# Kernel tuning notes

Hardware: AMD Instinct MI355X
Metric: run time of the kernel (lower is better)

## Reference

```python
import jax, jax.numpy as jnp
import numpy as np

NUM_HEADS = 16
HEAD_DIM = 64
MAX_TIME = 10000


def apply_rope(x):
    """Interleaved RoPE, faithful to apply_rotary_encoding with the _rope_kernel.

    The NxN kernel maps pairs (x0, x1) -> (-x1, x0); we do it with a reshape
    instead of the dense matmul for efficiency (same math).
    x: [b, t, h, d]
    """
    b, t, h, d = x.shape
    pos = jnp.arange(t, dtype=jnp.float32)                         # [t]
    freq_seq = jnp.arange(d // 2, dtype=jnp.float32) / (d // 2)
    inv_freq = jnp.repeat(jnp.float32(MAX_TIME) ** (-freq_seq), 2)  # [d], interleaved
    theta = pos[:, None] * inv_freq[None, :]                        # [t, d]
    pairs = x.reshape(b, t, h, d // 2, 2)
    x_rot = jnp.stack([-pairs[..., 1], pairs[..., 0]], axis=-1).reshape(b, t, h, d)
    cos = jnp.cos(theta).astype(x.dtype)[None, :, None, :]
    sin = jnp.sin(theta).astype(x.dtype)[None, :, None, :]
    return x * cos + x_rot * sin


def setup_inputs() -> dict:
    key = jax.random.key(0)
    ks = jax.random.split(key, 6)
    B, T, E = 8, 1024, 1024
    H = NUM_HEADS * HEAD_DIM
    s = 0.02  # typical init scale for bias-free Linear weights
    return {
        "inputs_q": jax.random.normal(ks[0], (B, T, E), jnp.float32),
        "inputs_kv": jax.random.normal(ks[1], (B, T, E), jnp.float32),
        "w_q": jax.random.normal(ks[2], (E, H), jnp.float32) * s,
        "w_k": jax.random.normal(ks[3], (E, H), jnp.float32) * s,
        "w_v": jax.random.normal(ks[4], (E, H), jnp.float32) * s,
        "w_o": jax.random.normal(ks[5], (H, E), jnp.float32) * s,
    }


def reference(inputs_q, inputs_kv, w_q, w_k, w_v, w_o):
    b, t, e = inputs_q.shape
    q = (inputs_q @ w_q).reshape(b, t, NUM_HEADS, HEAD_DIM)   # [b,t,h,d]
    k = (inputs_kv @ w_k).reshape(b, -1, NUM_HEADS, HEAD_DIM)  # [b,T,h,d]
    v = (inputs_kv @ w_v).reshape(b, -1, NUM_HEADS, HEAD_DIM)
    q = apply_rope(q)
    k = apply_rope(k)
    logits = jnp.einsum('bthd,bThd->bhtT', q, k) * (1.0 / jnp.sqrt(jnp.float32(HEAD_DIM)))
    attn = jax.nn.softmax(logits, axis=-1)                    # [b,h,t,T]
    out = jnp.einsum('bhtT,bThd->bthd', attn, v).reshape(b, t, NUM_HEADS * HEAD_DIM)
    return out @ w_o                                          # [b,t,e]
```

## Files before the change

kernel.cpp:

```cpp
#include <hip/hip_runtime.h>
#include <math.h>


typedef __attribute__((ext_vector_type(8))) short bf16x8;
typedef __attribute__((ext_vector_type(4))) float f32x4;
typedef __attribute__((ext_vector_type(16))) float f32x16;

#define LOG2E 1.44269504f
#define QSCALE (0.125f * LOG2E)

__device__ __forceinline__ ushort f2bf(float f) {
    union { float f; uint32_t u; } v; v.f = f;
    uint32_t r = (v.u + 0x7FFF + ((v.u >> 16) & 1)) >> 16;
    return (ushort)r;
}
__device__ __forceinline__ uint cvt_pk_bf16(float a, float b) {
    uint r;
    asm("v_cvt_pk_bf16_f32 %0, %1, %2" : "=v"(r) : "v"(a), "v"(b));
    return r;
}
__device__ __forceinline__ float bf2f(ushort u) {
    union { uint32_t u; float f; } v; v.u = ((uint32_t)u) << 16;
    return v.f;
}

__device__ __forceinline__ void gload16(const ushort* g, ushort* l) {
    __builtin_amdgcn_global_load_lds(
        (const __attribute__((address_space(1))) unsigned int*)g,
        (__attribute__((address_space(3))) unsigned int*)l, 16, 0, 0);
}

__global__ void prep(const float* __restrict__ xq,  ushort* __restrict__ Aq,
                     const float* __restrict__ xkv, ushort* __restrict__ Akv,
                     const float* __restrict__ wq,  ushort* __restrict__ WqT,
                     const float* __restrict__ wk,  ushort* __restrict__ WkT,
                     const float* __restrict__ wv,  ushort* __restrict__ WvT,
                     const float* __restrict__ wo,  ushort* __restrict__ WoT,
                     float2* __restrict__ tbl)
{
    __shared__ float t[32][33];
    const int bid = blockIdx.x;
    const int tid = threadIdx.x;

    if (bid < 8192) {
        const float* X = (bid < 4096) ? xq : xkv;
        ushort* Y = (bid < 4096) ? Aq : Akv;
        int i = (bid & 4095) * 256 + tid;
        float4 a = ((const float4*)X)[2 * i];
        float4 b = ((const float4*)X)[2 * i + 1];
        union { float4 f; ushort u[8]; } o;
        o.u[0] = f2bf(a.x); o.u[1] = f2bf(a.y); o.u[2] = f2bf(a.z); o.u[3] = f2bf(a.w);
        o.u[4] = f2bf(b.x); o.u[5] = f2bf(b.y); o.u[6] = f2bf(b.z); o.u[7] = f2bf(b.w);
        ((float4*)Y)[i] = o.f;
    } else if (bid < 12288) {
        int j = bid - 8192;
        int z = j >> 10, rem = j & 1023;
        const float* W = (z == 0) ? wq : (z == 1) ? wk : (z == 2) ? wv : wo;
        ushort* Wt = (z == 0) ? WqT : (z == 1) ? WkT : (z == 2) ? WvT : WoT;
        int bx = (rem & 31) * 32, by = (rem >> 5) * 32;
        int tx = tid & 31, ty = tid >> 5;
#pragma unroll
        for (int e = 0; e < 32; e += 8)
            t[ty + e][tx] = W[(size_t)(by + ty + e) * 1024 + bx + tx];
        __syncthreads();
#pragma unroll
        for (int e = 0; e < 32; e += 8)
            Wt[(size_t)(bx + ty + e) * 1024 + by + tx] = f2bf(t[tx][ty + e]);
    } else {
        int idx = (bid - 12288) * 256 + tid;
        int tt = idx >> 5, i = idx & 31;
        float inv_freq = exp2f(-(float)i * (13.28771238f / 32.0f));
        float s, c;
        sincosf((float)tt * inv_freq, &s, &c);
        tbl[idx] = make_float2(c, s);
    }
}

__global__ __launch_bounds__(256, 4)
void gemm_qkv(const ushort* __restrict__ Aq, const ushort* __restrict__ Akv,
              const ushort* __restrict__ Wt, ushort* __restrict__ Out,
              const float2* __restrict__ tbl)
{
    const int K = 1024, N = 1024;
    __shared__ ushort As[2][128 * 32];
    __shared__ ushort Bs[2][128 * 32];
    const int tid = threadIdx.x;
    const int w = tid >> 6, l = tid & 63;
    const int mat = blockIdx.y >> 3;
    const int row0 = blockIdx.x * 128, col0 = (blockIdx.y & 7) * 128;
    const int wr = (w >> 1) * 64, wc = (w & 1) * 64;

    const ushort* A = mat ? Akv : Aq;
    const ushort* Bt = Wt + (size_t)mat * (1024 * 1024);
    ushort* C = Out + (size_t)mat * 8388608;

    f32x4 acc[4][4];
#pragma unroll
    for (int i = 0; i < 4; ++i)
#pragma unroll
        for (int j = 0; j < 4; ++j) acc[i][j] = (f32x4)0.f;

    const ushort* Ag = A + (size_t)(row0 + w * 32 + (l >> 2)) * K + (l & 3) * 8;
    const ushort* Bg = Bt + (size_t)(col0 + w * 32 + (l >> 2)) * K + (l & 3) * 8;

    const int arow = (wr + (l & 15)) * 32;
    const int brow = (wc + (l & 15)) * 32;
    const int koff = (l >> 4) * 8;

    auto STAGE = [&](int buf, int kt) {
        ushort* Asw = &As[buf][w * 1024];
        ushort* Bsw = &Bs[buf][w * 1024];
        gload16(Ag + kt, Asw);
        gload16(Ag + 16 * K + kt, Asw + 512);
        gload16(Bg + kt, Bsw);
        gload16(Bg + 16 * K + kt, Bsw + 512);
    };
    auto COMPUTE = [&](int buf) {
        bf16x8 af[4], bfr[4];
#pragma unroll
        for (int fm = 0; fm < 4; ++fm)
            af[fm] = *(const bf16x8*)&As[buf][arow + fm * 512 + koff];
#pragma unroll
        for (int fn = 0; fn < 4; ++fn)
            bfr[fn] = *(const bf16x8*)&Bs[buf][brow + fn * 512 + koff];
#pragma unroll
        for (int fm = 0; fm < 4; ++fm)
#pragma unroll
            for (int fn = 0; fn < 4; ++fn)
                acc[fm][fn] = __builtin_amdgcn_mfma_f32_16x16x32_bf16(
                    af[fm], bfr[fn], acc[fm][fn], 0, 0, 0);
    };

    STAGE(0, 0);
    asm volatile("s_waitcnt vmcnt(0)" ::: "memory");
    __builtin_amdgcn_s_barrier();
    int cur = 0;
    for (int kt = 32; kt < K; kt += 32) {
        STAGE(cur ^ 1, kt);
        COMPUTE(cur);
        asm volatile("s_waitcnt vmcnt(0)" ::: "memory");
        __builtin_amdgcn_s_barrier();
        cur ^= 1;
    }
    COMPUTE(cur);

    const int crow = (l >> 4) * 4;
    const int ccol = l & 15;

    if (mat < 2) {
        const float scale = (mat == 0) ? QSCALE : 1.0f;
        const int odd = ccol & 1;
        int ipair[4];
#pragma unroll
        for (int fn = 0; fn < 4; ++fn)
            ipair[fn] = (fn * 16 + ccol) >> 1;
#pragma unroll
        for (int fm = 0; fm < 4; ++fm)
#pragma unroll
            for (int r = 0; r < 4; ++r) {
                int t = (row0 + wr + fm * 16 + crow + r) & 1023;
                const float2* tb = tbl + (t << 5);
#pragma unroll
                for (int fn = 0; fn < 4; ++fn) {
                    float x = acc[fm][fn][r];
                    float partner = __shfl_xor(x, 1, 64);
                    float2 cs = tb[ipair[fn]];
                    float o = odd ? fmaf(partner, cs.y, x * cs.x)
                                  : fmaf(-partner, cs.y, x * cs.x);
                    acc[fm][fn][r] = o * scale;
                }
            }
    }

#pragma unroll
    for (int fm = 0; fm < 4; ++fm)
#pragma unroll
        for (int fn = 0; fn < 4; ++fn)
#pragma unroll
            for (int r = 0; r < 4; ++r) {
                size_t row = row0 + wr + fm * 16 + crow + r;
                size_t col = col0 + wc + fn * 16 + ccol;
                C[row * N + col] = f2bf(acc[fm][fn][r]);
            }
}

__global__ __launch_bounds__(256, 2)
void gemm_out(const ushort* __restrict__ A, const ushort* __restrict__ Bt,
              float* __restrict__ C, int M, int N, int K)
{
    __shared__ ushort As[2][128 * 32];
    __shared__ ushort Bs[2][128 * 32];
    const int tid = threadIdx.x;
    const int w = tid >> 6, l = tid & 63;
    const int row0 = blockIdx.x * 128, col0 = blockIdx.y * 128;
    const int wr = (w >> 1) * 64, wc = (w & 1) * 64;

    f32x4 acc[4][4];
#pragma unroll
    for (int i = 0; i < 4; ++i)
#pragma unroll
        for (int j = 0; j < 4; ++j) acc[i][j] = (f32x4)0.f;

    const ushort* Ag = A + (size_t)(row0 + w * 32 + (l >> 2)) * K + (l & 3) * 8;
    const ushort* Bg = Bt + (size_t)(col0 + w * 32 + (l >> 2)) * K + (l & 3) * 8;

    const int arow = (wr + (l & 15)) * 32;
    const int brow = (wc + (l & 15)) * 32;
    const int koff = (l >> 4) * 8;

    auto STAGE = [&](int buf, int kt) {
        ushort* Asw = &As[buf][w * 1024];
        ushort* Bsw = &Bs[buf][w * 1024];
        gload16(Ag + kt, Asw);
        gload16(Ag + 16 * K + kt, Asw + 512);
        gload16(Bg + kt, Bsw);
        gload16(Bg + 16 * K + kt, Bsw + 512);
    };
    auto COMPUTE = [&](int buf) {
        bf16x8 af[4], bfr[4];
#pragma unroll
        for (int fm = 0; fm < 4; ++fm)
            af[fm] = *(const bf16x8*)&As[buf][arow + fm * 512 + koff];
#pragma unroll
        for (int fn = 0; fn < 4; ++fn)
            bfr[fn] = *(const bf16x8*)&Bs[buf][brow + fn * 512 + koff];
#pragma unroll
        for (int fm = 0; fm < 4; ++fm)
#pragma unroll
            for (int fn = 0; fn < 4; ++fn)
                acc[fm][fn] = __builtin_amdgcn_mfma_f32_16x16x32_bf16(
                    af[fm], bfr[fn], acc[fm][fn], 0, 0, 0);
    };

    STAGE(0, 0);
    asm volatile("s_waitcnt vmcnt(0)" ::: "memory");
    __builtin_amdgcn_s_barrier();
    int cur = 0;
    for (int kt = 32; kt < K; kt += 32) {
        STAGE(cur ^ 1, kt);
        COMPUTE(cur);
        asm volatile("s_waitcnt vmcnt(0)" ::: "memory");
        __builtin_amdgcn_s_barrier();
        cur ^= 1;
    }
    COMPUTE(cur);

    const int crow = (l >> 4) * 4;
    const int ccol = l & 15;
#pragma unroll
    for (int fm = 0; fm < 4; ++fm)
#pragma unroll
        for (int fn = 0; fn < 4; ++fn)
#pragma unroll
            for (int r = 0; r < 4; ++r) {
                size_t row = row0 + wr + fm * 16 + crow + r;
                size_t col = col0 + wc + fn * 16 + ccol;
                C[row * N + col] = acc[fm][fn][r];
            }
}

__global__ __launch_bounds__(256, 4)
void attn_bf16_v2(const ushort* __restrict__ Q, const ushort* __restrict__ K,
                  const ushort* __restrict__ V, ushort* __restrict__ O)
{
    __shared__ uint shm[4352];
    uint* Ksu = shm;
    uint* Vtu = shm + 2176;

    const int tid = threadIdx.x;
    const int w = tid >> 6, l = tid & 63;
    const int lo = l & 31, hi = l >> 5;
    const int bid = blockIdx.x;
    const int qt = bid >> 7;
    const int hb = bid & 127;
    const int h = hb >> 3, b = hb & 7;
    const int colh = h * 64;

    const size_t qrow = (size_t)(b * 1024 + qt * 128 + w * 32 + lo);
    bf16x8 qb[4];
#pragma unroll
    for (int kc = 0; kc < 4; ++kc)
        qb[kc] = *(const bf16x8*)&Q[qrow * 1024 + colh + kc * 16 + hi * 8];

    f32x16 acc[2];
#pragma unroll
    for (int i = 0; i < 2; ++i) acc[i] = (f32x16)0.f;
    float lsum = 0.f;

    const size_t kvbase = (size_t)b * 1024 * 1024 + colh;

    const int skey = tid >> 3, sc = tid & 7;
    const int kp = tid & 31, vg = tid >> 5;

    for (int kt = 0; kt < 16; ++kt) {
        __syncthreads();
#pragma unroll
        for (int u = 0; u < 2; ++u) {
            int key = skey + u * 32;
            uint4 kv = *(const uint4*)&K[kvbase + (size_t)(kt * 64 + key) * 1024 + sc * 8];
            *(uint2*)&Ksu[key * 34 + sc * 4] = make_uint2(kv.x, kv.y);
            *(uint2*)&Ksu[key * 34 + sc * 4 + 2] = make_uint2(kv.z, kv.w);
        }
        {
            uint4 va = *(const uint4*)&V[kvbase + (size_t)(kt * 64 + 2 * kp) * 1024 + vg * 8];
            uint4 vb = *(const uint4*)&V[kvbase + (size_t)(kt * 64 + 2 * kp + 1) * 1024 + vg * 8];
            const ushort* pa = (const ushort*)&va;
            const ushort* pb = (const ushort*)&vb;
#pragma unroll
            for (int e = 0; e < 8; ++e)
                Vtu[(vg * 8 + e) * 34 + kp] = (uint)pa[e] | ((uint)pb[e] << 16);
        }
        __syncthreads();

        uint pw[16];
#pragma unroll
        for (int mt = 0; mt < 2; ++mt) {
            f32x16 s = (f32x16)0.f;
            const int rbase = (mt * 32 + lo) * 34 + hi * 4;
#pragma unroll
            for (int kc = 0; kc < 4; ++kc) {
                union { uint2 d[2]; bf16x8 v; } ak;
                ak.d[0] = *(const uint2*)&Ksu[rbase + kc * 8];
                ak.d[1] = *(const uint2*)&Ksu[rbase + kc * 8 + 2];
                s = __builtin_amdgcn_mfma_f32_32x32x16_bf16(ak.v, qb[kc], s, 0, 0, 0);
            }
            float p[16];
#pragma unroll
            for (int r = 0; r < 16; ++r) {
                p[r] = exp2f(s[r]);
                lsum += p[r];
            }
#pragma unroll
            for (int rp = 0; rp < 8; ++rp)
                pw[mt * 8 + rp] = cvt_pk_bf16(p[2 * rp], p[2 * rp + 1]);
        }

        bf16x8 pf[4];
#pragma unroll
        for (int mt = 0; mt < 2; ++mt) {
            uint* W = &pw[mt * 8];
            uint e0 = (uint)__shfl_xor((int)(hi ? W[0] : W[2]), 32);
            uint e1 = (uint)__shfl_xor((int)(hi ? W[1] : W[3]), 32);
            uint e2 = (uint)__shfl_xor((int)(hi ? W[4] : W[6]), 32);
            uint e3 = (uint)__shfl_xor((int)(hi ? W[5] : W[7]), 32);
            union { uint u[4]; bf16x8 v; } f0, f1;
            if (hi == 0) {
                f0.u[0] = W[0]; f0.u[1] = W[1]; f0.u[2] = e0; f0.u[3] = e1;
                f1.u[0] = W[4]; f1.u[1] = W[5]; f1.u[2] = e2; f1.u[3] = e3;
            } else {
                f0.u[0] = e0; f0.u[1] = e1; f0.u[2] = W[2]; f0.u[3] = W[3];
                f1.u[0] = e2; f1.u[1] = e3; f1.u[2] = W[6]; f1.u[3] = W[7];
            }
            pf[mt * 2 + 0] = f0.v;
            pf[mt * 2 + 1] = f1.v;
        }

#pragma unroll
        for (int dmt = 0; dmt < 2; ++dmt) {
            const int rbase = (dmt * 32 + lo) * 34 + hi * 4;
#pragma unroll
            for (int kcg = 0; kcg < 4; ++kcg) {
                union { uint2 d[2]; bf16x8 v; } vk;
                vk.d[0] = *(const uint2*)&Vtu[rbase + kcg * 8];
                vk.d[1] = *(const uint2*)&Vtu[rbase + kcg * 8 + 2];
                acc[dmt] = __builtin_amdgcn_mfma_f32_32x32x16_bf16(vk.v, pf[kcg], acc[dmt], 0, 0, 0);
            }
        }
    }

    float tot = lsum + __shfl_xor(lsum, 32);
    float inv = 1.0f / tot;

    __syncthreads();
    uint* Osw = shm + w * 1056;
#pragma unroll
    for (int dmt = 0; dmt < 2; ++dmt)
#pragma unroll
        for (int rp = 0; rp < 8; ++rp) {
            float a0 = acc[dmt][2 * rp] * inv;
            float a1 = acc[dmt][2 * rp + 1] * inv;
            Osw[lo * 33 + dmt * 16 + (rp & 1) + 4 * (rp >> 1) + 2 * hi] =
                cvt_pk_bf16(a0, a1);
        }
    __builtin_amdgcn_s_waitcnt(0);
#pragma unroll
    for (int u = 0; u < 4; ++u) {
        int slot = l + u * 64;
        int qr = slot >> 3, c = slot & 7;
        float4 val = *(const float4*)&Osw[qr * 33 + c * 4];
        *(float4*)&O[(size_t)(b * 1024 + qt * 128 + w * 32 + qr) * 1024 + colh + c * 8] = val;
    }
}

extern "C" void kernel_launch(void* const* d_in, const int* in_sizes, int n_in,
                              void* d_out, int out_size, void* d_ws, size_t ws_size,
                              hipStream_t stream)
{
    const float* xq  = (const float*)d_in[0];
    const float* xkv = (const float*)d_in[1];
    const float* wq  = (const float*)d_in[2];
    const float* wk  = (const float*)d_in[3];
    const float* wv  = (const float*)d_in[4];
    const float* wo  = (const float*)d_in[5];
    float* out = (float*)d_out;

    const int M = 8192, N = 1024, Kd = 1024;
    ushort* Aq  = (ushort*)d_ws;
    ushort* Akv = Aq  + 8388608;
    ushort* WqT = Akv + 8388608;
    ushort* WkT = WqT + 1048576;
    ushort* WvT = WkT + 1048576;
    ushort* WoT = WvT + 1048576;
    ushort* Qb  = WoT + 1048576;
    ushort* Kb  = Qb  + 8388608;
    ushort* Vb  = Kb  + 8388608;
    ushort* Ob  = Vb  + 8388608;
    float2* Tbl = (float2*)(Ob + 8388608);

    prep<<<12416, 256, 0, stream>>>(xq, Aq, xkv, Akv, wq, WqT, wk, WkT,
                                    wv, WvT, wo, WoT, Tbl);

    gemm_qkv<<<dim3(64, 24), 256, 0, stream>>>(Aq, Akv, WqT, Qb, Tbl);

    attn_bf16_v2<<<1024, 256, 0, stream>>>(Qb, Kb, Vb, Ob);

    gemm_out<<<dim3(64, 8), 256, 0, stream>>>(Ob, WoT, out, M, N, Kd);
}
```

Baseline: 178.5 us.

## Double-buffer K/V tiles in attention kernel with register prefetch

The attention kernel now keeps two shared-memory buffers for the K and transposed-V tiles. It issues the global loads for the next tile before computing on the current one, then writes them to the alternate buffer afterwards. This hides global load latency behind the MFMA work and cuts the barriers per iteration from two to one. In exchange, shared memory per block doubles (about 34.8KB), which may cap occupancy at 4 blocks per CU, and register pressure rises from the prefetched values.

```diff
diff --git a/kernel.cpp b/kernel.cpp
--- a/kernel.cpp
+++ b/kernel.cpp
@@ -260,12 +260,10 @@
 }
 
 __global__ __launch_bounds__(256, 4)
-void attn_bf16_v2(const ushort* __restrict__ Q, const ushort* __restrict__ K,
+void attn_bf16_v3(const ushort* __restrict__ Q, const ushort* __restrict__ K,
                   const ushort* __restrict__ V, ushort* __restrict__ O)
 {
-    __shared__ uint shm[4352];
-    uint* Ksu = shm;
-    uint* Vtu = shm + 2176;
+    __shared__ uint shm[2][4352];
 
     const int tid = threadIdx.x;
     const int w = tid >> 6, l = tid & 63;
@@ -292,25 +290,43 @@
     const int skey = tid >> 3, sc = tid & 7;
     const int kp = tid & 31, vg = tid >> 5;
 
+    const ushort* Kg = &K[kvbase + (size_t)skey * 1024 + sc * 8];
+    const ushort* Vg = &V[kvbase + (size_t)(2 * kp) * 1024 + vg * 8];
+
+    {
+        uint4 k0 = *(const uint4*)Kg;
+        uint4 k1 = *(const uint4*)(Kg + 32 * 1024);
+        uint4 v0 = *(const uint4*)Vg;
+        uint4 v1 = *(const uint4*)(Vg + 1024);
+        uint* Ksu = shm[0];
+        uint* Vtu = shm[0] + 2176;
+        *(uint2*)&Ksu[skey * 34 + sc * 4]            = make_uint2(k0.x, k0.y);
+        *(uint2*)&Ksu[skey * 34 + sc * 4 + 2]        = make_uint2(k0.z, k0.w);
+        *(uint2*)&Ksu[(skey + 32) * 34 + sc * 4]     = make_uint2(k1.x, k1.y);
+        *(uint2*)&Ksu[(skey + 32) * 34 + sc * 4 + 2] = make_uint2(k1.z, k1.w);
+        const ushort* pa = (const ushort*)&v0;
+        const ushort* pb = (const ushort*)&v1;
+#pragma unroll
+        for (int e = 0; e < 8; ++e)
+            Vtu[(vg * 8 + e) * 34 + kp] = (uint)pa[e] | ((uint)pb[e] << 16);
+    }
+    __syncthreads();
+
+#pragma unroll 1
     for (int kt = 0; kt < 16; ++kt) {
-        __syncthreads();
-#pragma unroll
-        for (int u = 0; u < 2; ++u) {
-            int key = skey + u * 32;
-            uint4 kv = *(const uint4*)&K[kvbase + (size_t)(kt * 64 + key) * 1024 + sc * 8];
-            *(uint2*)&Ksu[key * 34 + sc * 4] = make_uint2(kv.x, kv.y);
-            *(uint2*)&Ksu[key * 34 + sc * 4 + 2] = make_uint2(kv.z, kv.w);
-        }
-        {
-            uint4 va = *(const uint4*)&V[kvbase + (size_t)(kt * 64 + 2 * kp) * 1024 + vg * 8];
-            uint4 vb = *(const uint4*)&V[kvbase + (size_t)(kt * 64 + 2 * kp + 1) * 1024 + vg * 8];
-            const ushort* pa = (const ushort*)&va;
-            const ushort* pb = (const ushort*)&vb;
-#pragma unroll
-            for (int e = 0; e < 8; ++e)
-                Vtu[(vg * 8 + e) * 34 + kp] = (uint)pa[e] | ((uint)pb[e] << 16);
-        }
-        __syncthreads();
+        const uint* Ksu = shm[kt & 1];
+        const uint* Vtu = shm[kt & 1] + 2176;
+        const bool more = (kt < 15);
+
+        uint4 nk0, nk1, nv0, nv1;
+        if (more) {
+            const ushort* Kn = Kg + (size_t)(kt + 1) * 64 * 1024;
+            const ushort* Vn = Vg + (size_t)(kt + 1) * 64 * 1024;
+            nk0 = *(const uint4*)Kn;
+            nk1 = *(const uint4*)(Kn + 32 * 1024);
+            nv0 = *(const uint4*)Vn;
+            nv1 = *(const uint4*)(Vn + 1024);
+        }
 
         uint pw[16];
 #pragma unroll
@@ -366,13 +382,27 @@
                 acc[dmt] = __builtin_amdgcn_mfma_f32_32x32x16_bf16(vk.v, pf[kcg], acc[dmt], 0, 0, 0);
             }
         }
+
+        if (more) {
+            uint* Kd = shm[(kt & 1) ^ 1];
+            uint* Vd = shm[(kt & 1) ^ 1] + 2176;
+            *(uint2*)&Kd[skey * 34 + sc * 4]            = make_uint2(nk0.x, nk0.y);
+            *(uint2*)&Kd[skey * 34 + sc * 4 + 2]        = make_uint2(nk0.z, nk0.w);
+            *(uint2*)&Kd[(skey + 32) * 34 + sc * 4]     = make_uint2(nk1.x, nk1.y);
+            *(uint2*)&Kd[(skey + 32) * 34 + sc * 4 + 2] = make_uint2(nk1.z, nk1.w);
+            const ushort* pa = (const ushort*)&nv0;
+            const ushort* pb = (const ushort*)&nv1;
+#pragma unroll
+            for (int e = 0; e < 8; ++e)
+                Vd[(vg * 8 + e) * 34 + kp] = (uint)pa[e] | ((uint)pb[e] << 16);
+        }
+        __syncthreads();
     }
 
     float tot = lsum + __shfl_xor(lsum, 32);
     float inv = 1.0f / tot;
 
-    __syncthreads();
-    uint* Osw = shm + w * 1056;
+    uint* Osw = shm[0] + w * 1056;
 #pragma unroll
     for (int dmt = 0; dmt < 2; ++dmt)
 #pragma unroll
@@ -422,7 +452,7 @@
 
     gemm_qkv<<<dim3(64, 24), 256, 0, stream>>>(Aq, Akv, WqT, Qb, Tbl);
 
-    attn_bf16_v2<<<1024, 256, 0, stream>>>(Qb, Kb, Vb, Ob);
+    attn_bf16_v3<<<1024, 256, 0, stream>>>(Qb, Kb, Vb, Ob);
 
     gemm_out<<<dim3(64, 8), 256, 0, stream>>>(Ob, WoT, out, M, N, Kd);
 }
```

New measurement: 206.9 us. 1.16x slower.
